# Optimization experiments

Hardware: AMD Instinct MI355X
Metric: run time of the kernel (lower is better)

The kernel has to match this reference:

```python
import jax, jax.numpy as jnp
import numpy as np

B = 262144          # batch of sample points
L = 16              # hash levels
T = 1 << 19         # hash table size per level
F = 2               # features per level
BASE_RES = 16
FINEST_RES = 512
DH = 64             # density MLP hidden
DOUT = 16           # density MLP out (density_out dim)
CH = 64             # color MLP hidden
PRIMES = np.array([1, 2654435761, 805459861], dtype=np.uint32)
_b = np.exp((np.log(FINEST_RES) - np.log(BASE_RES)) / (L - 1))
RES = jnp.asarray(np.floor(BASE_RES * _b ** np.arange(L)).astype(np.float32))  # (L,)


def _linear_init(key, fan_in, fan_out):
    kw, kb = jax.random.split(key)
    bound = 1.0 / np.sqrt(fan_in)
    w = jax.random.uniform(kw, (fan_in, fan_out), minval=-bound, maxval=bound)
    b = jax.random.uniform(kb, (fan_out,), minval=-bound, maxval=bound)
    return w, b


def setup_inputs() -> dict:
    key = jax.random.key(0)
    ks = jax.random.split(key, 10)
    coords = jax.random.uniform(ks[0], (B, 3), dtype=jnp.float32)          # in [0,1]
    directions = jax.random.normal(ks[1], (B, 3), dtype=jnp.float32)
    embeddings = jax.random.uniform(ks[2], (L, T, F), minval=-1e-4, maxval=1e-4, dtype=jnp.float32)
    dw1, db1 = _linear_init(ks[3], L * F, DH)
    dw2, db2 = _linear_init(ks[4], DH, DOUT)
    cw1, cb1 = _linear_init(ks[5], 16 + DOUT, CH)
    cw2, cb2 = _linear_init(ks[6], CH, CH)
    cw3, cb3 = _linear_init(ks[7], CH, CH)
    cw4, cb4 = _linear_init(ks[8], CH, 3)
    return dict(coords=coords, directions=directions, embeddings=embeddings,
                dw1=dw1, db1=db1, dw2=dw2, db2=db2,
                cw1=cw1, cb1=cb1, cw2=cw2, cb2=cb2,
                cw3=cw3, cb3=cb3, cw4=cw4, cb4=cb4)


def hash_encode(coords, embeddings):
    # coords: (B,3) in [0,1]; embeddings: (L,T,F)
    pos = coords[:, None, :] * RES[None, :, None]            # (B,L,3)
    p0 = jnp.floor(pos)
    frac = pos - p0                                           # (B,L,3)
    p0 = p0.astype(jnp.uint32)
    corners = jnp.stack([p0, p0 + jnp.uint32(1)], axis=-1)    # (B,L,3,2)
    h_ax = corners * jnp.asarray(PRIMES)[None, None, :, None]  # uint32 wraparound
    hidx = (h_ax[:, :, 0, :, None, None]
            ^ h_ax[:, :, 1, None, :, None]
            ^ h_ax[:, :, 2, None, None, :])                   # (B,L,2,2,2)
    hidx = (hidx & jnp.uint32(T - 1)).reshape(coords.shape[0], L, 8).astype(jnp.int32)
    feats = embeddings[jnp.arange(L)[None, :, None], hidx]    # (B,L,8,F)
    wx = jnp.stack([1.0 - frac[..., 0], frac[..., 0]], -1)    # (B,L,2)
    wy = jnp.stack([1.0 - frac[..., 1], frac[..., 1]], -1)
    wz = jnp.stack([1.0 - frac[..., 2], frac[..., 2]], -1)
    w = (wx[:, :, :, None, None] * wy[:, :, None, :, None] * wz[:, :, None, None, :])
    w = w.reshape(coords.shape[0], L, 8)                      # (B,L,8)
    out = jnp.sum(feats * w[..., None], axis=2)               # (B,L,F)
    return out.reshape(coords.shape[0], L * F)


def sh_encode_deg4(d):
    # d: (B,3) unit directions in [-1,1]; degree-4 real SH basis (16 comps)
    x, y, z = d[:, 0], d[:, 1], d[:, 2]
    xx, yy, zz = x * x, y * y, z * z
    xy, yz, xz = x * y, y * z, x * z
    c = jnp.full_like(x, 0.28209479177387814)
    return jnp.stack([
        c,
        -0.48860251190291987 * y,
        0.48860251190291987 * z,
        -0.48860251190291987 * x,
        1.0925484305920792 * xy,
        -1.0925484305920792 * yz,
        0.94617469575755997 * zz - 0.31539156525251999,
        -1.0925484305920792 * xz,
        0.54627421529603959 * (xx - yy),
        0.59004358992664352 * y * (-3.0 * xx + yy),
        2.8906114426405538 * xy * z,
        0.45704579946446572 * y * (1.0 - 5.0 * zz),
        0.3731763325901154 * z * (5.0 * zz - 3.0),
        0.45704579946446572 * x * (1.0 - 5.0 * zz),
        1.4453057213202769 * z * (xx - yy),
        0.59004358992664352 * x * (xx - 3.0 * yy),
    ], axis=1)


def reference(coords, directions, embeddings, dw1, db1, dw2, db2,
              cw1, cb1, cw2, cb2, cw3, cb3, cw4, cb4):
    # density net: hash encode -> Linear+ReLU -> Linear
    feat = hash_encode(coords, embeddings)                    # (B, L*F)
    h = jax.nn.relu(feat @ dw1 + db1)
    density_out = h @ dw2 + db2                               # (B, DOUT)
    density = jnp.exp(density_out[:, 0])                      # TruncExp fwd = exp
    # color net
    d = directions / jnp.linalg.norm(directions, axis=1, keepdims=True)
    d01 = (d + 1.0) / 2.0                                     # remap as in module
    sh = sh_encode_deg4(d01 * 2.0 - 1.0)                      # encoder maps back to [-1,1]
    inp = jnp.concatenate([sh, density_out], axis=1)          # (B, 32)
    x = jax.nn.relu(inp @ cw1 + cb1)
    x = jax.nn.relu(x @ cw2 + cb2)
    x = jax.nn.relu(x @ cw3 + cb3)
    color = jax.nn.sigmoid(x @ cw4 + cb4)                     # (B, 3)
    return density, color
```

## Files before the change

kernel.cpp:

```cpp
#include <hip/hip_runtime.h>
#include <cmath>

#define NPTS 262144
#define NLVL 16
#define TBL  524288u
#define TMASK 524287u
#define TPB  256
#define NQ   7

typedef __attribute__((ext_vector_type(8))) short short8;
typedef __attribute__((ext_vector_type(4))) float f32x4;

struct ResArr { float r[NLVL]; };
struct QuadInfo { int off[NQ]; int dim[NQ]; };

__device__ __forceinline__ unsigned short f2bf(float f) {
    union { float f; unsigned u; } v; v.f = f;
    unsigned r = v.u + 0x7FFFu + ((v.u >> 16) & 1u);
    return (unsigned short)(r >> 16);
}
__device__ __forceinline__ float blo(unsigned u) {
    union { unsigned v; float f; } x; x.v = u << 16; return x.f;
}
__device__ __forceinline__ float bhi(unsigned u) {
    union { unsigned v; float f; } x; x.v = u & 0xffff0000u; return x.f;
}
__device__ __forceinline__ unsigned packbf(float a, float b) {
    return (unsigned)f2bf(a) | ((unsigned)f2bf(b) << 16);
}

#define MFMA(a,b,c) __builtin_amdgcn_mfma_f32_16x16x32_bf16((a),(b),(c),0,0,0)

__global__ __launch_bounds__(256) void prep_k(
    const float* __restrict__ emb,
    uint4* __restrict__ quad, QuadInfo qi,
    const float* __restrict__ dw1, const float* __restrict__ db1,
    const float* __restrict__ dw2, const float* __restrict__ db2,
    const float* __restrict__ cw1, const float* __restrict__ cb1,
    const float* __restrict__ cw2, const float* __restrict__ cb2,
    const float* __restrict__ cw3, const float* __restrict__ cb3,
    const float* __restrict__ cw4, const float* __restrict__ cb4,
    unsigned short* __restrict__ wpk, float* __restrict__ bpk)
{
    const int l = blockIdx.y;
    const int tid = threadIdx.x;

    if (l == 7) {
        if (blockIdx.x != 0) return;
        const int wid  = tid >> 6;
        const int lane = tid & 63;
        const int m16  = lane & 15;
        const int q    = lane >> 4;
        const unsigned char MAT[28] = {0,0,0,0, 1,1, 2,2,2,2, 3,3,3,3,3,3,3,3, 4,4,4,4,4,4,4,4, 5,5};
        const unsigned char K0 [28] = {0,0,0,0, 0,32, 0,0,0,0, 0,0,0,0,32,32,32,32, 0,0,0,0,32,32,32,32, 0,32};
        const unsigned char N0 [28] = {0,16,32,48, 0,0, 0,16,32,48, 0,16,32,48,0,16,32,48, 0,16,32,48,0,16,32,48, 0,0};
        #pragma unroll
        for (int s = 0; s < 28; ++s) {
            if ((s & 3) == wid) {
                const int mat = MAT[s];
                const float* src = mat==0?dw1 : mat==1?dw2 : mat==2?cw1 : mat==3?cw2 : mat==4?cw3 : cw4;
                const int fan = (mat==1) ? 16 : (mat==5) ? 3 : 64;
                const int k = (int)K0[s] + q*8;
                const int n = (int)N0[s] + m16;
                unsigned short u[8];
                #pragma unroll
                for (int j = 0; j < 8; ++j) {
                    float v = 0.f;
                    if (mat != 5 || n < 3) v = src[(k+j)*fan + n];
                    u[j] = f2bf(v);
                }
                unsigned* w32 = (unsigned*)(wpk + s*512 + lane*8);
                w32[0] = (unsigned)u[0] | ((unsigned)u[1] << 16);
                w32[1] = (unsigned)u[2] | ((unsigned)u[3] << 16);
                w32[2] = (unsigned)u[4] | ((unsigned)u[5] << 16);
                w32[3] = (unsigned)u[6] | ((unsigned)u[7] << 16);
            }
        }
        {
            int t = tid;
            if      (t <  64) bpk[t] = db1[t];
            else if (t <  80) bpk[t] = db2[t-64];
            else if (t < 144) bpk[t] = cb1[t-80];
            else if (t < 208) bpk[t] = cb2[t-144];
        }
        if (tid < 80) {
            int t = tid + 208;
            if (t < 272) bpk[t] = cb3[t-208];
            else         bpk[t] = (t-272 < 3) ? cb4[t-272] : 0.f;
        }
        return;
    }

    const int t = blockIdx.x * 256 + tid;
    const int D = qi.dim[l];
    if (t >= D*D*D) return;
    const unsigned z = (unsigned)t % (unsigned)D;
    const unsigned rem = (unsigned)t / (unsigned)D;
    const unsigned y = rem % (unsigned)D;
    const unsigned x = rem / (unsigned)D;

    const float2* __restrict__ emb2 = (const float2*)emb;
    const unsigned base = (unsigned)l * TBL;
    const unsigned hy0 = y*2654435761u, hy1 = (y+1u)*2654435761u;
    const unsigned hz0 = z*805459861u,  hz1 = (z+1u)*805459861u;

    const float2 a = emb2[base + ((x^hy0^hz0)&TMASK)];
    const float2 b = emb2[base + ((x^hy0^hz1)&TMASK)];
    const float2 c = emb2[base + ((x^hy1^hz0)&TMASK)];
    const float2 d = emb2[base + ((x^hy1^hz1)&TMASK)];

    uint4 q;
    q.x = packbf(a.x, a.y);
    q.y = packbf(b.x, b.y);
    q.z = packbf(c.x, c.y);
    q.w = packbf(d.x, d.y);
    quad[qi.off[l] + t] = q;
}

__global__ __launch_bounds__(256) void hash_encode_k(
    const float* __restrict__ coords,
    const float* __restrict__ emb,
    const uint4* __restrict__ quad,
    unsigned* __restrict__ featws,
    ResArr res, QuadInfo qi)
{
    const int tid = threadIdx.x;
    const int b   = blockIdx.x;
    const int xcd = b & 7;
    const int s   = b >> 3;

    if (s < 1152) {
        int l, p;
        if (s < 1024) {
            l = 7 + xcd;
            p = s * 256 + tid;
        } else {
            l = 15;
            p = xcd * 32768 + (s - 1024) * 256 + tid;
        }

        const float cx = coords[3*p], cy = coords[3*p+1], cz = coords[3*p+2];
        const float r = res.r[l];
        const float px = cx*r, py = cy*r, pz = cz*r;
        const float fpx = floorf(px), fpy = floorf(py), fpz = floorf(pz);
        const float fx = px-fpx, fy = py-fpy, fz = pz-fpz;
        const unsigned ix=(unsigned)fpx, iy=(unsigned)fpy, iz=(unsigned)fpz;
        const unsigned hx0=ix,             hx1=ix+1u;
        const unsigned hy0=iy*2654435761u, hy1=(iy+1u)*2654435761u;
        const unsigned hz0=iz*805459861u,  hz1=(iz+1u)*805459861u;
        const unsigned base = (unsigned)l * TBL;
        const float2* __restrict__ emb2 = (const float2*)emb;

        const float2 f000 = emb2[base + ((hx0^hy0^hz0)&TMASK)];
        const float2 f001 = emb2[base + ((hx0^hy0^hz1)&TMASK)];
        const float2 f010 = emb2[base + ((hx0^hy1^hz0)&TMASK)];
        const float2 f011 = emb2[base + ((hx0^hy1^hz1)&TMASK)];
        const float2 f100 = emb2[base + ((hx1^hy0^hz0)&TMASK)];
        const float2 f101 = emb2[base + ((hx1^hy0^hz1)&TMASK)];
        const float2 f110 = emb2[base + ((hx1^hy1^hz0)&TMASK)];
        const float2 f111 = emb2[base + ((hx1^hy1^hz1)&TMASK)];

        const float wx0=1.f-fx, wy0=1.f-fy, wz0=1.f-fz;
        float o0, o1;
        o0 = wx0*wy0*wz0*f000.x;                 o1 = wx0*wy0*wz0*f000.y;
        o0 = fmaf(wx0*wy0*fz,  f001.x, o0);      o1 = fmaf(wx0*wy0*fz,  f001.y, o1);
        o0 = fmaf(wx0*fy*wz0,  f010.x, o0);      o1 = fmaf(wx0*fy*wz0,  f010.y, o1);
        o0 = fmaf(wx0*fy*fz,   f011.x, o0);      o1 = fmaf(wx0*fy*fz,   f011.y, o1);
        o0 = fmaf(fx*wy0*wz0,  f100.x, o0);      o1 = fmaf(fx*wy0*wz0,  f100.y, o1);
        o0 = fmaf(fx*wy0*fz,   f101.x, o0);      o1 = fmaf(fx*wy0*fz,   f101.y, o1);
        o0 = fmaf(fx*fy*wz0,   f110.x, o0);      o1 = fmaf(fx*fy*wz0,   f110.y, o1);
        o0 = fmaf(fx*fy*fz,    f111.x, o0);      o1 = fmaf(fx*fy*fz,    f111.y, o1);

        featws[(size_t)l * NPTS + p] = packbf(o0, o1);
    } else {
        const int g  = xcd * 224 + (s - 1152);
        const int l  = g >> 8;
        const int c  = g & 255;
        const int D  = qi.dim[l];
        const int DD = D*D;
        const int off = qi.off[l];
        const float r = res.r[l];

        int   pidx[4];
        uint4 qA[4], qB[4];
        float fxa[4], fya[4], fza[4];
        #pragma unroll
        for (int k = 0; k < 4; ++k) {
            const int p = c*1024 + k*256 + tid;
            pidx[k] = p;
            const float cx = coords[3*p], cy = coords[3*p+1], cz = coords[3*p+2];
            const float px = cx*r, py = cy*r, pz = cz*r;
            const float fpx = floorf(px), fpy = floorf(py), fpz = floorf(pz);
            fxa[k] = px-fpx; fya[k] = py-fpy; fza[k] = pz-fpz;
            const int ix=(int)fpx, iy=(int)fpy, iz=(int)fpz;
            const int v0 = off + (ix*D + iy)*D + iz;
            qA[k] = quad[v0];
            qB[k] = quad[v0 + DD];
        }
        #pragma unroll
        for (int k = 0; k < 4; ++k) {
            const float fx = fxa[k], fy = fya[k], fz = fza[k];
            const float wx0=1.f-fx, wy0=1.f-fy, wz0=1.f-fz;
            const float w000=wx0*wy0*wz0, w001=wx0*wy0*fz;
            const float w010=wx0*fy*wz0,  w011=wx0*fy*fz;
            const float w100=fx*wy0*wz0,  w101=fx*wy0*fz;
            const float w110=fx*fy*wz0,   w111=fx*fy*fz;
            float o0, o1;
            o0 = w000*blo(qA[k].x);              o1 = w000*bhi(qA[k].x);
            o0 = fmaf(w001, blo(qA[k].y), o0);   o1 = fmaf(w001, bhi(qA[k].y), o1);
            o0 = fmaf(w010, blo(qA[k].z), o0);   o1 = fmaf(w010, bhi(qA[k].z), o1);
            o0 = fmaf(w011, blo(qA[k].w), o0);   o1 = fmaf(w011, bhi(qA[k].w), o1);
            o0 = fmaf(w100, blo(qB[k].x), o0);   o1 = fmaf(w100, bhi(qB[k].x), o1);
            o0 = fmaf(w101, blo(qB[k].y), o0);   o1 = fmaf(w101, bhi(qB[k].y), o1);
            o0 = fmaf(w110, blo(qB[k].z), o0);   o1 = fmaf(w110, bhi(qB[k].z), o1);
            o0 = fmaf(w111, blo(qB[k].w), o0);   o1 = fmaf(w111, bhi(qB[k].w), o1);
            featws[(size_t)l * NPTS + pidx[k]] = packbf(o0, o1);
        }
    }
}

__global__ __launch_bounds__(256, 2) void mlp_mfma_k(
    const unsigned* __restrict__ featws,
    const unsigned short* __restrict__ wpk,
    const float* __restrict__ bpk,
    const float* __restrict__ dirs,
    float* __restrict__ out)
{
    const int tid  = threadIdx.x;
    const int wid  = tid >> 6;
    const int lane = tid & 63;
    const int m16  = lane & 15;
    const int q    = lane >> 4;

    __shared__ __align__(16) unsigned short wlds[28 * 512];
    __shared__ float blds[288];
    __shared__ __align__(16) unsigned short featL[TPB * 40];
    __shared__ __align__(16) unsigned short actL[4 * 16 * 72];

    {
        uint4* dst = (uint4*)wlds;
        const uint4* srcv = (const uint4*)wpk;
        #pragma unroll
        for (int j = 0; j < 7; ++j) dst[j*256 + tid] = srcv[j*256 + tid];
        if (tid < 256) blds[tid] = bpk[tid];
        if (tid < 32)  blds[256 + tid] = bpk[256 + tid];
    }

    const int pbase = blockIdx.x * TPB;
    unsigned* fL32 = (unsigned*)featL;
    #pragma unroll
    for (int j = 0; j < 16; ++j) {
        const int idx  = j*256 + tid;
        const int l    = idx >> 8;
        const int ploc = idx & 255;
        fL32[ploc*20 + l] = featws[(size_t)l * NPTS + pbase + ploc];
    }
    __syncthreads();

    unsigned short* aw = actL + wid*1152;
    const short8* wfr = (const short8*)wlds;

    #pragma unroll
    for (int iter = 0; iter < 4; ++iter) {
        const int tile = wid + 4*iter;
        const int loc0 = tile*16;
        const int p0g  = pbase + loc0;

        short8 a0 = *(const short8*)(featL + (loc0+m16)*40 + q*8);
        f32x4 acc[4];
        #pragma unroll
        for (int nc = 0; nc < 4; ++nc) {
            const float b = blds[nc*16 + m16];
            acc[nc] = (f32x4){b,b,b,b};
            acc[nc] = MFMA(a0, wfr[nc*64 + lane], acc[nc]);
        }
        #pragma unroll
        for (int nc = 0; nc < 4; ++nc)
            #pragma unroll
            for (int r = 0; r < 4; ++r)
                aw[(q*4+r)*72 + nc*16 + m16] = f2bf(fmaxf(acc[nc][r], 0.f));

        short8 ad0 = *(const short8*)(aw + m16*72 + q*8);
        short8 ad1 = *(const short8*)(aw + m16*72 + 32 + q*8);
        f32x4 dob;
        { const float b = blds[64 + m16]; dob = (f32x4){b,b,b,b}; }
        dob = MFMA(ad0, wfr[4*64 + lane], dob);
        dob = MFMA(ad1, wfr[5*64 + lane], dob);

        if (m16 == 0) {
            #pragma unroll
            for (int r = 0; r < 4; ++r) out[p0g + q*4 + r] = expf(dob[r]);
        }

        #pragma unroll
        for (int r = 0; r < 4; ++r)
            aw[(q*4+r)*72 + 16 + m16] = f2bf(dob[r]);
        {
            const int pg = p0g + m16;
            const float dx0 = dirs[3*pg], dy0 = dirs[3*pg+1], dz0 = dirs[3*pg+2];
            const float inv = 1.f / sqrtf(dx0*dx0 + dy0*dy0 + dz0*dz0);
            float x = dx0*inv, y = dy0*inv, z = dz0*inv;
            x = ((x+1.f)*0.5f)*2.f - 1.f;
            y = ((y+1.f)*0.5f)*2.f - 1.f;
            z = ((z+1.f)*0.5f)*2.f - 1.f;
            float s0, s1, s2, s3;
            switch (q) {
            case 0: s0 = 0.28209479177387814f;
                    s1 = -0.48860251190291987f*y;
                    s2 =  0.48860251190291987f*z;
                    s3 = -0.48860251190291987f*x; break;
            case 1: s0 =  1.0925484305920792f*x*y;
                    s1 = -1.0925484305920792f*y*z;
                    s2 =  0.94617469575756f*z*z - 0.31539156525252f;
                    s3 = -1.0925484305920792f*x*z; break;
            case 2: s0 =  0.5462742152960396f*(x*x - y*y);
                    s1 =  0.5900435899266435f*y*(-3.f*x*x + y*y);
                    s2 =  2.890611442640554f*x*y*z;
                    s3 =  0.4570457994644657f*y*(1.f - 5.f*z*z); break;
            default:s0 =  0.3731763325901154f*z*(5.f*z*z - 3.f);
                    s1 =  0.4570457994644657f*x*(1.f - 5.f*z*z);
                    s2 =  1.445305721320277f*z*(x*x - y*y);
                    s3 =  0.5900435899266435f*x*(x*x - 3.f*y*y); break;
            }
            unsigned* ip = (unsigned*)(aw + m16*72 + q*4);
            ip[0] = packbf(s0, s1);
            ip[1] = packbf(s2, s3);
        }

        short8 ac0 = *(const short8*)(aw + m16*72 + q*8);
        #pragma unroll
        for (int nc = 0; nc < 4; ++nc) {
            const float b = blds[80 + nc*16 + m16];
            acc[nc] = (f32x4){b,b,b,b};
            acc[nc] = MFMA(ac0, wfr[(6+nc)*64 + lane], acc[nc]);
        }
        #pragma unroll
        for (int nc = 0; nc < 4; ++nc)
            #pragma unroll
            for (int r = 0; r < 4; ++r)
                aw[(q*4+r)*72 + nc*16 + m16] = f2bf(fmaxf(acc[nc][r], 0.f));

        short8 a20 = *(const short8*)(aw + m16*72 + q*8);
        short8 a21 = *(const short8*)(aw + m16*72 + 32 + q*8);
        #pragma unroll
        for (int nc = 0; nc < 4; ++nc) {
            const float b = blds[144 + nc*16 + m16];
            acc[nc] = (f32x4){b,b,b,b};
            acc[nc] = MFMA(a20, wfr[(10+nc)*64 + lane], acc[nc]);
            acc[nc] = MFMA(a21, wfr[(14+nc)*64 + lane], acc[nc]);
        }
        #pragma unroll
        for (int nc = 0; nc < 4; ++nc)
            #pragma unroll
            for (int r = 0; r < 4; ++r)
                aw[(q*4+r)*72 + nc*16 + m16] = f2bf(fmaxf(acc[nc][r], 0.f));

        short8 a30 = *(const short8*)(aw + m16*72 + q*8);
        short8 a31 = *(const short8*)(aw + m16*72 + 32 + q*8);
        #pragma unroll
        for (int nc = 0; nc < 4; ++nc) {
            const float b = blds[208 + nc*16 + m16];
            acc[nc] = (f32x4){b,b,b,b};
            acc[nc] = MFMA(a30, wfr[(18+nc)*64 + lane], acc[nc]);
            acc[nc] = MFMA(a31, wfr[(22+nc)*64 + lane], acc[nc]);
        }
        #pragma unroll
        for (int nc = 0; nc < 4; ++nc)
            #pragma unroll
            for (int r = 0; r < 4; ++r)
                aw[(q*4+r)*72 + nc*16 + m16] = f2bf(fmaxf(acc[nc][r], 0.f));

        short8 a40 = *(const short8*)(aw + m16*72 + q*8);
        short8 a41 = *(const short8*)(aw + m16*72 + 32 + q*8);
        f32x4 c4;
        { const float b = blds[272 + m16]; c4 = (f32x4){b,b,b,b}; }
        c4 = MFMA(a40, wfr[26*64 + lane], c4);
        c4 = MFMA(a41, wfr[27*64 + lane], c4);
        if (m16 < 3) {
            #pragma unroll
            for (int r = 0; r < 4; ++r)
                out[NPTS + 3*(p0g + q*4 + r) + m16] = 1.f / (1.f + expf(-c4[r]));
        }
    }
}

extern "C" void kernel_launch(void* const* d_in, const int* in_sizes, int n_in,
                              void* d_out, int out_size, void* d_ws, size_t ws_size,
                              hipStream_t stream)
{
    ResArr res;
    const double b = exp((log(512.0) - log(16.0)) / 15.0);
    for (int l = 0; l < NLVL; ++l)
        res.r[l] = (float)floor(16.0 * pow(b, (double)l));

    QuadInfo qi;
    int off = 0, maxn = 0;
    for (int l = 0; l < NQ; ++l) {
        const int D = (int)res.r[l] + 1;
        qi.dim[l] = D;
        qi.off[l] = off;
        off += D*D*D;
        if (D*D*D > maxn) maxn = D*D*D;
    }

    unsigned*       featws = (unsigned*)d_ws;
    uint4*          quad   = (uint4*)((char*)d_ws + (size_t)NLVL * NPTS * 4);
    unsigned short* wpk    = (unsigned short*)((char*)quad + (size_t)off * 16);
    float*          bpk    = (float*)((char*)wpk + 28 * 512 * 2);

    prep_k<<<dim3((maxn + 255)/256, 8), 256, 0, stream>>>(
        (const float*)d_in[2], quad, qi,
        (const float*)d_in[3],  (const float*)d_in[4],
        (const float*)d_in[5],  (const float*)d_in[6],
        (const float*)d_in[7],  (const float*)d_in[8],
        (const float*)d_in[9],  (const float*)d_in[10],
        (const float*)d_in[11], (const float*)d_in[12],
        (const float*)d_in[13], (const float*)d_in[14],
        wpk, bpk);

    hash_encode_k<<<11008, 256, 0, stream>>>(
        (const float*)d_in[0],
        (const float*)d_in[2],
        quad, featws, res, qi);

    mlp_mfma_k<<<NPTS/TPB, 256, 0, stream>>>(
        featws, wpk, bpk,
        (const float*)d_in[1],
        (float*)d_out);
}
```

Measured before the change: 253.7 us.

## Interleave quad pairs into octet layout and pad coords to float4

The prep kernel now writes each quad entry both to its own slot and as the second half of the entry one x-slice lower. A dense-level lookup can then fetch both corner quads from adjacent 32-byte memory instead of two locations DD apart. Coordinates are also repacked into an aligned float4 buffer so the hash kernel does one vector load instead of three strided scalar loads. The cost is doubled dense-table storage, extra write traffic in prep, and an extra coordinate copy pass.

```diff
diff --git a/kernel.cpp b/kernel.cpp
--- a/kernel.cpp
+++ b/kernel.cpp
@@ -33,7 +33,9 @@
 
 __global__ __launch_bounds__(256) void prep_k(
     const float* __restrict__ emb,
-    uint4* __restrict__ quad, QuadInfo qi,
+    const float* __restrict__ coords,
+    float4* __restrict__ c4,
+    uint4* __restrict__ oct, QuadInfo qi,
     const float* __restrict__ dw1, const float* __restrict__ db1,
     const float* __restrict__ dw2, const float* __restrict__ db2,
     const float* __restrict__ cw1, const float* __restrict__ cb1,
@@ -46,47 +48,53 @@
     const int tid = threadIdx.x;
 
     if (l == 7) {
-        if (blockIdx.x != 0) return;
-        const int wid  = tid >> 6;
-        const int lane = tid & 63;
-        const int m16  = lane & 15;
-        const int q    = lane >> 4;
-        const unsigned char MAT[28] = {0,0,0,0, 1,1, 2,2,2,2, 3,3,3,3,3,3,3,3, 4,4,4,4,4,4,4,4, 5,5};
-        const unsigned char K0 [28] = {0,0,0,0, 0,32, 0,0,0,0, 0,0,0,0,32,32,32,32, 0,0,0,0,32,32,32,32, 0,32};
-        const unsigned char N0 [28] = {0,16,32,48, 0,0, 0,16,32,48, 0,16,32,48,0,16,32,48, 0,16,32,48,0,16,32,48, 0,0};
-        #pragma unroll
-        for (int s = 0; s < 28; ++s) {
-            if ((s & 3) == wid) {
-                const int mat = MAT[s];
-                const float* src = mat==0?dw1 : mat==1?dw2 : mat==2?cw1 : mat==3?cw2 : mat==4?cw3 : cw4;
-                const int fan = (mat==1) ? 16 : (mat==5) ? 3 : 64;
-                const int k = (int)K0[s] + q*8;
-                const int n = (int)N0[s] + m16;
-                unsigned short u[8];
-                #pragma unroll
-                for (int j = 0; j < 8; ++j) {
-                    float v = 0.f;
-                    if (mat != 5 || n < 3) v = src[(k+j)*fan + n];
-                    u[j] = f2bf(v);
+        if (blockIdx.x == 0) {
+            const int wid  = tid >> 6;
+            const int lane = tid & 63;
+            const int m16  = lane & 15;
+            const int q    = lane >> 4;
+            const unsigned char MAT[28] = {0,0,0,0, 1,1, 2,2,2,2, 3,3,3,3,3,3,3,3, 4,4,4,4,4,4,4,4, 5,5};
+            const unsigned char K0 [28] = {0,0,0,0, 0,32, 0,0,0,0, 0,0,0,0,32,32,32,32, 0,0,0,0,32,32,32,32, 0,32};
+            const unsigned char N0 [28] = {0,16,32,48, 0,0, 0,16,32,48, 0,16,32,48,0,16,32,48, 0,16,32,48,0,16,32,48, 0,0};
+            #pragma unroll
+            for (int s = 0; s < 28; ++s) {
+                if ((s & 3) == wid) {
+                    const int mat = MAT[s];
+                    const float* src = mat==0?dw1 : mat==1?dw2 : mat==2?cw1 : mat==3?cw2 : mat==4?cw3 : cw4;
+                    const int fan = (mat==1) ? 16 : (mat==5) ? 3 : 64;
+                    const int k = (int)K0[s] + q*8;
+                    const int n = (int)N0[s] + m16;
+                    unsigned short u[8];
+                    #pragma unroll
+                    for (int j = 0; j < 8; ++j) {
+                        float v = 0.f;
+                        if (mat != 5 || n < 3) v = src[(k+j)*fan + n];
+                        u[j] = f2bf(v);
+                    }
+                    unsigned* w32 = (unsigned*)(wpk + s*512 + lane*8);
+                    w32[0] = (unsigned)u[0] | ((unsigned)u[1] << 16);
+                    w32[1] = (unsigned)u[2] | ((unsigned)u[3] << 16);
+                    w32[2] = (unsigned)u[4] | ((unsigned)u[5] << 16);
+                    w32[3] = (unsigned)u[6] | ((unsigned)u[7] << 16);
                 }
-                unsigned* w32 = (unsigned*)(wpk + s*512 + lane*8);
-                w32[0] = (unsigned)u[0] | ((unsigned)u[1] << 16);
-                w32[1] = (unsigned)u[2] | ((unsigned)u[3] << 16);
-                w32[2] = (unsigned)u[4] | ((unsigned)u[5] << 16);
-                w32[3] = (unsigned)u[6] | ((unsigned)u[7] << 16);
             }
-        }
-        {
-            int t = tid;
-            if      (t <  64) bpk[t] = db1[t];
-            else if (t <  80) bpk[t] = db2[t-64];
-            else if (t < 144) bpk[t] = cb1[t-80];
-            else if (t < 208) bpk[t] = cb2[t-144];
-        }
-        if (tid < 80) {
-            int t = tid + 208;
-            if (t < 272) bpk[t] = cb3[t-208];
-            else         bpk[t] = (t-272 < 3) ? cb4[t-272] : 0.f;
+            {
+                int t = tid;
+                if      (t <  64) bpk[t] = db1[t];
+                else if (t <  80) bpk[t] = db2[t-64];
+                else if (t < 144) bpk[t] = cb1[t-80];
+                else if (t < 208) bpk[t] = cb2[t-144];
+            }
+            if (tid < 80) {
+                int t = tid + 208;
+                if (t < 272) bpk[t] = cb3[t-208];
+                else         bpk[t] = (t-272 < 3) ? cb4[t-272] : 0.f;
+            }
+        } else if (blockIdx.x <= 1024) {
+            const int p = (blockIdx.x - 1) * 256 + tid;
+            float4 c;
+            c.x = coords[3*p]; c.y = coords[3*p+1]; c.z = coords[3*p+2]; c.w = 0.f;
+            c4[p] = c;
         }
         return;
     }
@@ -94,13 +102,14 @@
     const int t = blockIdx.x * 256 + tid;
     const int D = qi.dim[l];
     if (t >= D*D*D) return;
+    const int DD = D*D;
     const unsigned z = (unsigned)t % (unsigned)D;
     const unsigned rem = (unsigned)t / (unsigned)D;
     const unsigned y = rem % (unsigned)D;
-    const unsigned x = rem / (unsigned)D;
 
     const float2* __restrict__ emb2 = (const float2*)emb;
     const unsigned base = (unsigned)l * TBL;
+    const unsigned x = rem / (unsigned)D;
     const unsigned hy0 = y*2654435761u, hy1 = (y+1u)*2654435761u;
     const unsigned hz0 = z*805459861u,  hz1 = (z+1u)*805459861u;
 
@@ -114,13 +123,17 @@
     q.y = packbf(b.x, b.y);
     q.z = packbf(c.x, c.y);
     q.w = packbf(d.x, d.y);
-    quad[qi.off[l] + t] = q;
+
+    const int e = qi.off[l] + t;
+    oct[2*e] = q;
+    if (t >= DD)
+        oct[2*(e - DD) + 1] = q;
 }
 
 __global__ __launch_bounds__(256) void hash_encode_k(
-    const float* __restrict__ coords,
+    const float4* __restrict__ c4,
     const float* __restrict__ emb,
-    const uint4* __restrict__ quad,
+    const uint4* __restrict__ oct,
     unsigned* __restrict__ featws,
     ResArr res, QuadInfo qi)
 {
@@ -139,9 +152,9 @@
             p = xcd * 32768 + (s - 1024) * 256 + tid;
         }
 
-        const float cx = coords[3*p], cy = coords[3*p+1], cz = coords[3*p+2];
+        const float4 cc = c4[p];
         const float r = res.r[l];
-        const float px = cx*r, py = cy*r, pz = cz*r;
+        const float px = cc.x*r, py = cc.y*r, pz = cc.z*r;
         const float fpx = floorf(px), fpy = floorf(py), fpz = floorf(pz);
         const float fx = px-fpx, fy = py-fpy, fz = pz-fpz;
         const unsigned ix=(unsigned)fpx, iy=(unsigned)fpy, iz=(unsigned)fpz;
@@ -177,7 +190,6 @@
         const int l  = g >> 8;
         const int c  = g & 255;
         const int D  = qi.dim[l];
-        const int DD = D*D;
         const int off = qi.off[l];
         const float r = res.r[l];
 
@@ -188,14 +200,14 @@
         for (int k = 0; k < 4; ++k) {
             const int p = c*1024 + k*256 + tid;
             pidx[k] = p;
-            const float cx = coords[3*p], cy = coords[3*p+1], cz = coords[3*p+2];
-            const float px = cx*r, py = cy*r, pz = cz*r;
+            const float4 cc = c4[p];
+            const float px = cc.x*r, py = cc.y*r, pz = cc.z*r;
             const float fpx = floorf(px), fpy = floorf(py), fpz = floorf(pz);
             fxa[k] = px-fpx; fya[k] = py-fpy; fza[k] = pz-fpz;
             const int ix=(int)fpx, iy=(int)fpy, iz=(int)fpz;
             const int v0 = off + (ix*D + iy)*D + iz;
-            qA[k] = quad[v0];
-            qB[k] = quad[v0 + DD];
+            qA[k] = oct[2*v0];
+            qB[k] = oct[2*v0 + 1];
         }
         #pragma unroll
         for (int k = 0; k < 4; ++k) {
@@ -372,14 +384,14 @@
 
         short8 a40 = *(const short8*)(aw + m16*72 + q*8);
         short8 a41 = *(const short8*)(aw + m16*72 + 32 + q*8);
-        f32x4 c4;
-        { const float b = blds[272 + m16]; c4 = (f32x4){b,b,b,b}; }
-        c4 = MFMA(a40, wfr[26*64 + lane], c4);
-        c4 = MFMA(a41, wfr[27*64 + lane], c4);
+        f32x4 c4v;
+        { const float b = blds[272 + m16]; c4v = (f32x4){b,b,b,b}; }
+        c4v = MFMA(a40, wfr[26*64 + lane], c4v);
+        c4v = MFMA(a41, wfr[27*64 + lane], c4v);
         if (m16 < 3) {
             #pragma unroll
             for (int r = 0; r < 4; ++r)
-                out[NPTS + 3*(p0g + q*4 + r) + m16] = 1.f / (1.f + expf(-c4[r]));
+                out[NPTS + 3*(p0g + q*4 + r) + m16] = 1.f / (1.f + expf(-c4v[r]));
         }
     }
 }
@@ -404,12 +416,15 @@
     }
 
     unsigned*       featws = (unsigned*)d_ws;
-    uint4*          quad   = (uint4*)((char*)d_ws + (size_t)NLVL * NPTS * 4);
-    unsigned short* wpk    = (unsigned short*)((char*)quad + (size_t)off * 16);
+    uint4*          oct    = (uint4*)((char*)d_ws + (size_t)NLVL * NPTS * 4);
+    float4*         c4     = (float4*)((char*)oct + (size_t)off * 32);
+    unsigned short* wpk    = (unsigned short*)((char*)c4 + (size_t)NPTS * 16);
     float*          bpk    = (float*)((char*)wpk + 28 * 512 * 2);
 
     prep_k<<<dim3((maxn + 255)/256, 8), 256, 0, stream>>>(
-        (const float*)d_in[2], quad, qi,
+        (const float*)d_in[2],
+        (const float*)d_in[0],
+        c4, oct, qi,
         (const float*)d_in[3],  (const float*)d_in[4],
         (const float*)d_in[5],  (const float*)d_in[6],
         (const float*)d_in[7],  (const float*)d_in[8],
@@ -419,9 +434,9 @@
         wpk, bpk);
 
     hash_encode_k<<<11008, 256, 0, stream>>>(
-        (const float*)d_in[0],
+        c4,
         (const float*)d_in[2],
-        quad, featws, res, qi);
+        oct, featws, res, qi);
 
     mlp_mfma_k<<<NPTS/TPB, 256, 0, stream>>>(
         featws, wpk, bpk,
```

Result: slower. 258.8 us (+2.0%).
